# Performance work log

Hardware: AMD Instinct MI355X
Metric: run time of the kernel (lower is better)

Reference implementation:

```python
import jax, jax.numpy as jnp
import numpy as np

B, S, F, T = 32, 512, 512, 1024  # batch, seq_len(channel dim), feat_dim, time length


def setup_inputs() -> dict:
    key = jax.random.key(0)
    ks = jax.random.split(key, 6)
    scale = 0.05  # keep tanh/softmax in a non-saturated regime
    return {
        "z_robot": jax.random.normal(ks[0], (B, S, T), dtype=jnp.float32),
        "z_human": jax.random.normal(ks[1], (B, S, T), dtype=jnp.float32),
        "W_b": jax.random.normal(ks[2], (S, S), dtype=jnp.float32) * scale,
        "W_q": jax.random.normal(ks[3], (F, S), dtype=jnp.float32) * scale,
        "W_v": jax.random.normal(ks[4], (F, S), dtype=jnp.float32) * scale,
        "w_hq": jax.random.normal(ks[5], (1, F), dtype=jnp.float32) * scale,
    }


def reference(z_robot, z_human, W_b, W_q, W_v, w_hq):
    # aux = W_b @ z_human : [B, S, Th]
    aux = jnp.einsum('su,buh->bsh', W_b, z_human)
    # C = tanh(z_robot^T @ aux) : [B, Tr, Th]
    C = jnp.tanh(jnp.einsum('bst,bsh->bth', z_robot, aux))
    # aux2 = W_v @ z_human : [B, F, Th];  aux3 = W_q @ z_robot : [B, F, Tr]
    aux2 = jnp.einsum('fs,bsh->bfh', W_v, z_human)
    aux3 = jnp.einsum('fs,bst->bft', W_q, z_robot)
    # H_q = tanh(aux3 + aux2 @ C^T) : [B, F, Tr]
    H_q = jnp.tanh(aux3 + jnp.einsum('bfh,bth->bft', aux2, C))
    # a_q = softmax(w_hq @ H_q, axis=2) : [B, 1, Tr]
    a_q = jax.nn.softmax(jnp.einsum('of,bft->bot', w_hq, H_q), axis=2)
    # attn = z_robot @ a_q^T : [B, S, 1]
    attn = jnp.einsum('bst,bot->bso', z_robot, a_q)
    return (attn, a_q, C)
```

## Files before the change

### kernel.cpp

```cpp
#include <hip/hip_runtime.h>
#include <math.h>


using f32x4  = __attribute__((ext_vector_type(4))) float;
using bf16x8 = __attribute__((ext_vector_type(8))) short;

__device__ __forceinline__ ushort f2bf(float x) {
    uint u = __float_as_uint(x);
    return (ushort)((u + 0x7fffu + ((u >> 16) & 1u)) >> 16);
}
__device__ __forceinline__ float bf2f(ushort h) { return __uint_as_float((uint)h << 16); }

__device__ __forceinline__ float fast_tanh(float x) {
    return 1.0f - 2.0f / (__expf(2.0f * x) + 1.0f);
}

__device__ __forceinline__ void gll16(const void* g, void* l) {
    __builtin_amdgcn_global_load_lds(
        (__attribute__((address_space(1))) void*)(void*)g,
        (__attribute__((address_space(3))) void*)l, 16, 0, 0);
}


__global__ __launch_bounds__(256)
void transpose_split_k(const float* __restrict__ in, ushort* __restrict__ hi,
                       ushort* __restrict__ lo, int R, int Cn) {
    __shared__ float tile[32][33];
    const int b = blockIdx.z;
    const float* inb = in + (size_t)b * R * Cn;
    const int c0 = blockIdx.x * 32, r0 = blockIdx.y * 32;
    const int tx = threadIdx.x, ty = threadIdx.y;
    #pragma unroll
    for (int i = 0; i < 32; i += 8)
        tile[ty + i][tx] = inb[(size_t)(r0 + ty + i) * Cn + c0 + tx];
    __syncthreads();
    const size_t ob = (size_t)b * R * Cn;
    #pragma unroll
    for (int i = 0; i < 32; i += 8) {
        const float v = tile[tx][ty + i];
        const ushort h = f2bf(v);
        const size_t o = ob + (size_t)(c0 + ty + i) * R + r0 + tx;
        hi[o] = h;
        lo[o] = f2bf(v - bf2f(h));
    }
}

__global__ __launch_bounds__(256)
void convert_split_k(const float* __restrict__ in, ushort* __restrict__ hi,
                     ushort* __restrict__ lo, int n) {
    const int i = blockIdx.x * 256 + threadIdx.x;
    if (i < n) {
        const float v = in[i];
        const ushort h = f2bf(v);
        hi[i] = h;
        if (lo) lo[i] = f2bf(v - bf2f(h));
    }
}

template <int MODE>
__global__ __launch_bounds__(256, 2)
void gemm_split(const ushort* __restrict__ Ahi, const ushort* __restrict__ Alo,
                long sAb, int ldA,
                const ushort* __restrict__ Bhi, const ushort* __restrict__ Blo,
                long sBb, int ldB, int K,
                ushort* __restrict__ Ohi, ushort* __restrict__ Olo,
                float* __restrict__ Of, ushort* __restrict__ O16,
                int ldO, long sOb) {
    __shared__ __align__(16) ushort lds[32768];
    const int b = blockIdx.z, m0 = blockIdx.y * 128, n0 = blockIdx.x * 128;
    const int t = threadIdx.x, l = t & 63, w = t >> 6, wm = w >> 1, wn = w & 1;

    const int srow = l >> 2;
    const int sch  = ((l & 3) ^ (srow & 3)) * 8;
    const ushort* pAh = Ahi + (long)b * sAb + (long)(m0 + w * 32 + srow) * ldA + sch;
    const ushort* pAl = Alo + (long)b * sAb + (long)(m0 + w * 32 + srow) * ldA + sch;
    const ushort* pBh = Bhi + (long)b * sBb + (long)(n0 + w * 32 + srow) * ldB + sch;
    const ushort* pBl = Blo + (long)b * sBb + (long)(n0 + w * 32 + srow) * ldB + sch;

    const int q = l >> 4;
    int offA[4], offB[4];
    #pragma unroll
    for (int i = 0; i < 4; ++i) {
        const int rA = wm * 64 + i * 16 + (l & 15);
        offA[i] = rA * 32 + (q ^ (rA & 3)) * 8;
        const int rB = wn * 64 + i * 16 + (l & 15);
        offB[i] = rB * 32 + (q ^ (rB & 3)) * 8;
    }

    auto stage = [&](int k0, int st) {
        const int base = st * 16384;
        #pragma unroll
        for (int tt = 0; tt < 2; ++tt) {
            const int lo_ = base + (w * 32 + tt * 16) * 32;
            gll16(pAh + (long)(tt * 16) * ldA + k0, lds + lo_);
            gll16(pAl + (long)(tt * 16) * ldA + k0, lds + 4096 + lo_);
            gll16(pBh + (long)(tt * 16) * ldB + k0, lds + 8192 + lo_);
            gll16(pBl + (long)(tt * 16) * ldB + k0, lds + 12288 + lo_);
        }
    };

    f32x4 acc[4][4] = {};
    stage(0, 0);
    int st = 0;
    for (int k0 = 0; k0 < K; k0 += 32) {
        __syncthreads();
        if (k0 + 32 < K) stage(k0 + 32, st ^ 1);
        const int base = st * 16384;
        bf16x8 ah[4], al4[4], bh[4], bl4[4];
        #pragma unroll
        for (int i = 0; i < 4; ++i) {
            ah[i]  = *(const bf16x8*)&lds[base + offA[i]];
            al4[i] = *(const bf16x8*)&lds[base + 4096 + offA[i]];
            bh[i]  = *(const bf16x8*)&lds[base + 8192 + offB[i]];
            bl4[i] = *(const bf16x8*)&lds[base + 12288 + offB[i]];
        }
        #pragma unroll
        for (int i = 0; i < 4; ++i)
            #pragma unroll
            for (int j = 0; j < 4; ++j) {
                acc[i][j] = __builtin_amdgcn_mfma_f32_16x16x32_bf16(ah[i],  bh[j],  acc[i][j], 0, 0, 0);
                acc[i][j] = __builtin_amdgcn_mfma_f32_16x16x32_bf16(ah[i],  bl4[j], acc[i][j], 0, 0, 0);
                acc[i][j] = __builtin_amdgcn_mfma_f32_16x16x32_bf16(al4[i], bh[j],  acc[i][j], 0, 0, 0);
            }
        st ^= 1;
    }

    const int cl = l & 15, rl = (l >> 4) * 4;
    #pragma unroll
    for (int i = 0; i < 4; ++i)
        #pragma unroll
        for (int r = 0; r < 4; ++r) {
            const long mg = m0 + wm * 64 + i * 16 + rl + r;
            #pragma unroll
            for (int j = 0; j < 4; ++j) {
                const int ng = n0 + wn * 64 + j * 16 + cl;
                const float v = acc[i][j][r];
                const long o = (long)b * sOb + mg * ldO + ng;
                if (MODE == 0) {
                    const ushort h = f2bf(v);
                    Ohi[o] = h;
                    Olo[o] = f2bf(v - bf2f(h));
                } else {
                    const float tv = fast_tanh(v);
                    Of[o] = tv;
                    O16[o] = f2bf(tv);
                }
            }
        }
}

__device__ __forceinline__ void plain_core(
    const ushort* __restrict__ A, long sAb, int ldA,
    const ushort* __restrict__ B, long sBb, int ldB, int K,
    int b, int m0, int n0, ushort* lds, f32x4 (&acc)[4][4]) {
    const int t = threadIdx.x, l = t & 63, w = t >> 6, wm = w >> 1, wn = w & 1;
    const int srow = l >> 3;
    const int sch  = ((l & 7) ^ (srow & 7)) * 8;
    const ushort* pA = A + (long)b * sAb + (long)(m0 + w * 32 + srow) * ldA + sch;
    const ushort* pB = B + (long)b * sBb + (long)(n0 + w * 32 + srow) * ldB + sch;
    const int q = l >> 4;
    int offA[4], offB[4];
    #pragma unroll
    for (int i = 0; i < 4; ++i) {
        const int rA = wm * 64 + i * 16 + (l & 15);
        offA[i] = rA * 64 + (q ^ (rA & 7)) * 8;
        const int rB = wn * 64 + i * 16 + (l & 15);
        offB[i] = 8192 + rB * 64 + (q ^ (rB & 7)) * 8;
    }
    auto stage = [&](int k0, int st) {
        const int base = st * 16384;
        #pragma unroll
        for (int tt = 0; tt < 4; ++tt) {
            gll16(pA + (long)(tt * 8) * ldA + k0, lds + base + (w * 32 + tt * 8) * 64);
            gll16(pB + (long)(tt * 8) * ldB + k0, lds + base + 8192 + (w * 32 + tt * 8) * 64);
        }
    };
    stage(0, 0);
    int st = 0;
    for (int k0 = 0; k0 < K; k0 += 64) {
        __syncthreads();
        if (k0 + 64 < K) stage(k0 + 64, st ^ 1);
        const int base = st * 16384;
        #pragma unroll
        for (int s = 0; s < 2; ++s) {
            bf16x8 av[4], bv[4];
            #pragma unroll
            for (int i = 0; i < 4; ++i) {
                av[i] = *(const bf16x8*)&lds[base + (offA[i] ^ (s * 32))];
                bv[i] = *(const bf16x8*)&lds[base + (offB[i] ^ (s * 32))];
            }
            #pragma unroll
            for (int i = 0; i < 4; ++i)
                #pragma unroll
                for (int j = 0; j < 4; ++j)
                    acc[i][j] = __builtin_amdgcn_mfma_f32_16x16x32_bf16(av[i], bv[j], acc[i][j], 0, 0, 0);
        }
        st ^= 1;
    }
    __syncthreads();
}

__global__ __launch_bounds__(256, 2)
void gemm_plain_store(const ushort* __restrict__ A, long sAb, int ldA,
                      const ushort* __restrict__ B, long sBb, int ldB, int K,
                      ushort* __restrict__ O, long sOb, int ldO) {
    __shared__ __align__(16) ushort lds[32768];
    const int b = blockIdx.z, m0 = blockIdx.y * 128, n0 = blockIdx.x * 128;
    f32x4 acc[4][4] = {};
    plain_core(A, sAb, ldA, B, sBb, ldB, K, b, m0, n0, lds, acc);
    const int t = threadIdx.x, l = t & 63, w = t >> 6, wm = w >> 1, wn = w & 1;
    const int cl = l & 15, rl = (l >> 4) * 4;
    #pragma unroll
    for (int i = 0; i < 4; ++i)
        #pragma unroll
        for (int r = 0; r < 4; ++r) {
            const long mg = m0 + wm * 64 + i * 16 + rl + r;
            #pragma unroll
            for (int j = 0; j < 4; ++j)
                O[(long)b * sOb + mg * ldO + n0 + wn * 64 + j * 16 + cl] = f2bf(acc[i][j][r]);
        }
}

__global__ __launch_bounds__(256, 2)
void gemm_fused_logits(const ushort* __restrict__ Wq16, const ushort* __restrict__ zrT,
                       const ushort* __restrict__ aux2, const ushort* __restrict__ C16,
                       const float* __restrict__ whq, float* __restrict__ logits) {
    __shared__ __align__(16) ushort lds[32768];
    const int b = blockIdx.z, m0 = blockIdx.y * 128, n0 = blockIdx.x * 128;
    f32x4 acc[4][4] = {};
    plain_core(Wq16, 0, 512, zrT, 524288, 512, 512, b, m0, n0, lds, acc);
    plain_core(aux2, 524288, 1024, C16, 1048576, 1024, 1024, b, m0, n0, lds, acc);
    const int t = threadIdx.x, l = t & 63, w = t >> 6, wm = w >> 1, wn = w & 1;
    float p[4] = {0.f, 0.f, 0.f, 0.f};
    #pragma unroll
    for (int i = 0; i < 4; ++i)
        #pragma unroll
        for (int r = 0; r < 4; ++r) {
            const float wv = whq[m0 + wm * 64 + i * 16 + (l >> 4) * 4 + r];
            #pragma unroll
            for (int j = 0; j < 4; ++j)
                p[j] += wv * fast_tanh(acc[i][j][r]);
        }
    #pragma unroll
    for (int j = 0; j < 4; ++j) {
        p[j] += __shfl_xor(p[j], 16);
        p[j] += __shfl_xor(p[j], 32);
    }
    float* red = (float*)lds;
    if (l < 16) {
        #pragma unroll
        for (int j = 0; j < 4; ++j)
            red[wm * 128 + wn * 64 + j * 16 + l] = p[j];
    }
    __syncthreads();
    if (t < 128)
        atomicAdd(&logits[(long)b * 1024 + n0 + t], red[t] + red[128 + t]);
}

__global__ __launch_bounds__(256)
void softmax_kernel(const float* __restrict__ logits, float* __restrict__ aq, int T) {
    __shared__ float sm[256];
    const int b = blockIdx.x, tid = threadIdx.x;
    float v[4];
    float mx = -1e30f;
    #pragma unroll
    for (int i = 0; i < 4; ++i) {
        v[i] = logits[(size_t)b * T + tid + 256 * i];
        mx = fmaxf(mx, v[i]);
    }
    sm[tid] = mx; __syncthreads();
    for (int s = 128; s > 0; s >>= 1) {
        if (tid < s) sm[tid] = fmaxf(sm[tid], sm[tid + s]);
        __syncthreads();
    }
    mx = sm[0]; __syncthreads();
    float e[4], sum = 0.f;
    #pragma unroll
    for (int i = 0; i < 4; ++i) { e[i] = __expf(v[i] - mx); sum += e[i]; }
    sm[tid] = sum; __syncthreads();
    for (int s = 128; s > 0; s >>= 1) {
        if (tid < s) sm[tid] += sm[tid + s];
        __syncthreads();
    }
    const float inv = 1.0f / sm[0];
    #pragma unroll
    for (int i = 0; i < 4; ++i)
        aq[(size_t)b * T + tid + 256 * i] = e[i] * inv;
}

__global__ __launch_bounds__(256)
void attn_kernel(const float* __restrict__ ZR, const float* __restrict__ aq,
                 float* __restrict__ out, int S, int T) {
    const int b = blockIdx.y;
    const int s = blockIdx.x * 4 + (threadIdx.x >> 6);
    const int lane = threadIdx.x & 63;
    const float* row = ZR + ((size_t)b * S + s) * T;
    const float* a = aq + (size_t)b * T;
    float sum = 0.f;
    for (int t = lane; t < T; t += 64) sum += row[t] * a[t];
    #pragma unroll
    for (int off = 32; off > 0; off >>= 1) sum += __shfl_down(sum, off, 64);
    if (lane == 0) out[(size_t)b * S + s] = sum;
}

#define BM 64
#define BN 64
#define BK 16
#define PAD 4

__global__ __launch_bounds__(256)
void gemm_nn(const float* __restrict__ A, const float* __restrict__ Bm,
             float* __restrict__ D, int M, int N, int K) {
    __shared__ float As[BK][BM + PAD];
    __shared__ float Bs[BK][BN + PAD];
    const int b = blockIdx.z, m0 = blockIdx.y * BM, n0 = blockIdx.x * BN;
    const int tx = threadIdx.x, ty = threadIdx.y, f = ty * 16 + tx;
    const float* Bb = Bm + (size_t)b * K * N;
    float acc[4][4] = {};
    const int ka = f % 16, ma = f / 16, nb = f % 64, kb = f / 64;
    for (int k0 = 0; k0 < K; k0 += BK) {
        #pragma unroll
        for (int i = 0; i < 4; ++i)
            As[ka][ma + 16 * i] = A[(size_t)(m0 + ma + 16 * i) * K + k0 + ka];
        #pragma unroll
        for (int i = 0; i < 4; ++i)
            Bs[kb + 4 * i][nb] = Bb[(size_t)(k0 + kb + 4 * i) * N + n0 + nb];
        __syncthreads();
        #pragma unroll
        for (int k = 0; k < BK; ++k) {
            float av[4], bv[4];
            *(float4*)av = *(const float4*)&As[k][ty * 4];
            *(float4*)bv = *(const float4*)&Bs[k][tx * 4];
            #pragma unroll
            for (int i = 0; i < 4; ++i)
                #pragma unroll
                for (int j = 0; j < 4; ++j) acc[i][j] += av[i] * bv[j];
        }
        __syncthreads();
    }
    float* Db = D + (size_t)b * M * N;
    #pragma unroll
    for (int i = 0; i < 4; ++i)
        *(float4*)&Db[(size_t)(m0 + ty * 4 + i) * N + n0 + tx * 4] =
            make_float4(acc[i][0], acc[i][1], acc[i][2], acc[i][3]);
}

__global__ __launch_bounds__(256)
void gemm_tn_tanh(const float* __restrict__ ZR, const float* __restrict__ AUX,
                  float* __restrict__ C, int M, int N, int K) {
    __shared__ float As[BK][BM + PAD];
    __shared__ float Bs[BK][BN + PAD];
    const int b = blockIdx.z, m0 = blockIdx.y * BM, n0 = blockIdx.x * BN;
    const int tx = threadIdx.x, ty = threadIdx.y, f = ty * 16 + tx;
    const float* ZRb = ZR + (size_t)b * K * M;
    const float* AUXb = AUX + (size_t)b * K * N;
    float acc[4][4] = {};
    const int nl = f % 64, kl = f / 64;
    for (int k0 = 0; k0 < K; k0 += BK) {
        #pragma unroll
        for (int i = 0; i < 4; ++i)
            As[kl + 4 * i][nl] = ZRb[(size_t)(k0 + kl + 4 * i) * M + m0 + nl];
        #pragma unroll
        for (int i = 0; i < 4; ++i)
            Bs[kl + 4 * i][nl] = AUXb[(size_t)(k0 + kl + 4 * i) * N + n0 + nl];
        __syncthreads();
        #pragma unroll
        for (int k = 0; k < BK; ++k) {
            float av[4], bv[4];
            *(float4*)av = *(const float4*)&As[k][ty * 4];
            *(float4*)bv = *(const float4*)&Bs[k][tx * 4];
            #pragma unroll
            for (int i = 0; i < 4; ++i)
                #pragma unroll
                for (int j = 0; j < 4; ++j) acc[i][j] += av[i] * bv[j];
        }
        __syncthreads();
    }
    float* Cb = C + (size_t)b * M * N;
    #pragma unroll
    for (int i = 0; i < 4; ++i)
        *(float4*)&Cb[(size_t)(m0 + ty * 4 + i) * N + n0 + tx * 4] =
            make_float4(fast_tanh(acc[i][0]), fast_tanh(acc[i][1]),
                        fast_tanh(acc[i][2]), fast_tanh(acc[i][3]));
}

__global__ __launch_bounds__(256)
void gemm_nt_fused(const float* __restrict__ Wq, const float* __restrict__ ZR,
                   const float* __restrict__ A2, const float* __restrict__ Cm,
                   const float* __restrict__ whq, float* __restrict__ logits,
                   int M, int N, int K1, int K2) {
    __shared__ float As[BK][BM + PAD];
    __shared__ float Bs[BK][BN + PAD];
    __shared__ float red[16][BN];
    const int b = blockIdx.z, m0 = blockIdx.y * BM, n0 = blockIdx.x * BN;
    const int tx = threadIdx.x, ty = threadIdx.y, f = ty * 16 + tx;
    const float* ZRb = ZR + (size_t)b * K1 * N;
    const float* A2b = A2 + (size_t)b * M * K2;
    const float* Cb = Cm + (size_t)b * N * K2;
    float acc3[4][4] = {};
    {
        const int ka = f % 16, ma = f / 16, nb = f % 64, kb = f / 64;
        for (int k0 = 0; k0 < K1; k0 += BK) {
            #pragma unroll
            for (int i = 0; i < 4; ++i)
                As[ka][ma + 16 * i] = Wq[(size_t)(m0 + ma + 16 * i) * K1 + k0 + ka];
            #pragma unroll
            for (int i = 0; i < 4; ++i)
                Bs[kb + 4 * i][nb] = ZRb[(size_t)(k0 + kb + 4 * i) * N + n0 + nb];
            __syncthreads();
            #pragma unroll
            for (int k = 0; k < BK; ++k) {
                float av[4], bv[4];
                *(float4*)av = *(const float4*)&As[k][ty * 4];
                *(float4*)bv = *(const float4*)&Bs[k][tx * 4];
                #pragma unroll
                for (int i = 0; i < 4; ++i)
                    #pragma unroll
                    for (int j = 0; j < 4; ++j) acc3[i][j] += av[i] * bv[j];
            }
            __syncthreads();
        }
    }
    float acc[4][4] = {};
    {
        const int ka = f % 16, ra = f / 16;
        for (int k0 = 0; k0 < K2; k0 += BK) {
            #pragma unroll
            for (int i = 0; i < 4; ++i)
                As[ka][ra + 16 * i] = A2b[(size_t)(m0 + ra + 16 * i) * K2 + k0 + ka];
            #pragma unroll
            for (int i = 0; i < 4; ++i)
                Bs[ka][ra + 16 * i] = Cb[(size_t)(n0 + ra + 16 * i) * K2 + k0 + ka];
            __syncthreads();
            #pragma unroll
            for (int k = 0; k < BK; ++k) {
                float av[4], bv[4];
                *(float4*)av = *(const float4*)&As[k][ty * 4];
                *(float4*)bv = *(const float4*)&Bs[k][tx * 4];
                #pragma unroll
                for (int i = 0; i < 4; ++i)
                    #pragma unroll
                    for (int j = 0; j < 4; ++j) acc[i][j] += av[i] * bv[j];
            }
            __syncthreads();
        }
    }
    float p[4] = {0.f, 0.f, 0.f, 0.f};
    #pragma unroll
    for (int i = 0; i < 4; ++i) {
        const float wv = whq[m0 + ty * 4 + i];
        #pragma unroll
        for (int j = 0; j < 4; ++j) p[j] += wv * fast_tanh(acc3[i][j] + acc[i][j]);
    }
    #pragma unroll
    for (int j = 0; j < 4; ++j) red[ty][tx * 4 + j] = p[j];
    __syncthreads();
    if (f < BN) {
        float s = 0.f;
        #pragma unroll
        for (int r = 0; r < 16; ++r) s += red[r][f];
        atomicAdd(&logits[(size_t)b * N + n0 + f], s);
    }
}

extern "C" void kernel_launch(void* const* d_in, const int* in_sizes, int n_in,
                              void* d_out, int out_size, void* d_ws, size_t ws_size,
                              hipStream_t stream) {
    const float* z_robot = (const float*)d_in[0];
    const float* z_human = (const float*)d_in[1];
    const float* W_b     = (const float*)d_in[2];
    const float* W_q     = (const float*)d_in[3];
    const float* W_v     = (const float*)d_in[4];
    const float* w_hq    = (const float*)d_in[5];
    float* out = (float*)d_out;

    const int Bn = 32, S = 512, F = 512, T = 1024;
    float* attn_out = out;
    float* aq_out   = out + (size_t)Bn * S;
    float* C_out    = out + (size_t)Bn * S + (size_t)Bn * T;

    char* ws = (char*)d_ws;
    const size_t E2 = 33554432;

    ushort* zhT_hi  = (ushort*)(ws);
    ushort* zhT_lo  = (ushort*)(ws + E2);
    ushort* zrT_hi  = (ushort*)(ws + 2 * E2);
    ushort* zrT_lo  = (ushort*)(ws + 3 * E2);
    ushort* auxT_hi = (ushort*)(ws + 4 * E2);
    ushort* auxT_lo = (ushort*)(ws + 5 * E2);
    ushort* C16     = (ushort*)(ws + 6 * E2);
    ushort* aux2    = auxT_hi;
    ushort* Wb_hi   = (ushort*)(ws + 8 * E2);
    ushort* Wb_lo   = Wb_hi + 262144;
    ushort* Wq16    = Wb_hi + 524288;
    ushort* Wv16    = Wb_hi + 786432;
    float*  logitsF = (float*)(ws + 8 * E2 + 2097152);
    const size_t FAST_REQ = 8 * E2 + 2097152 + 131072;

    if (ws_size >= FAST_REQ) {
        hipMemsetAsync(logitsF, 0, (size_t)Bn * T * sizeof(float), stream);
        transpose_split_k<<<dim3(32, 16, Bn), dim3(32, 8), 0, stream>>>(z_human, zhT_hi, zhT_lo, 512, 1024);
        transpose_split_k<<<dim3(32, 16, Bn), dim3(32, 8), 0, stream>>>(z_robot, zrT_hi, zrT_lo, 512, 1024);
        convert_split_k<<<dim3(1024), dim3(256), 0, stream>>>(W_b, Wb_hi, Wb_lo, 262144);
        convert_split_k<<<dim3(1024), dim3(256), 0, stream>>>(W_q, Wq16, nullptr, 262144);
        convert_split_k<<<dim3(1024), dim3(256), 0, stream>>>(W_v, Wv16, nullptr, 262144);
        gemm_split<0><<<dim3(4, 8, Bn), dim3(256), 0, stream>>>(
            zhT_hi, zhT_lo, 524288, 512, Wb_hi, Wb_lo, 0, 512, 512,
            auxT_hi, auxT_lo, nullptr, nullptr, 512, 524288);
        gemm_split<1><<<dim3(8, 8, Bn), dim3(256), 0, stream>>>(
            zrT_hi, zrT_lo, 524288, 512, auxT_hi, auxT_lo, 524288, 512, 512,
            nullptr, nullptr, C_out, C16, 1024, 1048576);
        gemm_plain_store<<<dim3(8, 4, Bn), dim3(256), 0, stream>>>(
            Wv16, 0, 512, zhT_hi, 524288, 512, 512, aux2, 524288, 1024);
        gemm_fused_logits<<<dim3(8, 4, Bn), dim3(256), 0, stream>>>(
            Wq16, zrT_hi, aux2, C16, w_hq, logitsF);
        softmax_kernel<<<dim3(Bn), dim3(256), 0, stream>>>(logitsF, aq_out, T);
        attn_kernel<<<dim3(S / 4, Bn), dim3(256), 0, stream>>>(z_robot, aq_out, attn_out, S, T);
    } else {
        float* ws0    = (float*)ws;
        float* logits = (float*)(ws + (size_t)Bn * S * T * 4);
        hipMemsetAsync(logits, 0, (size_t)Bn * T * sizeof(float), stream);
        dim3 blk(16, 16);
        gemm_nn<<<dim3(T / BN, S / BM, Bn), blk, 0, stream>>>(W_b, z_human, ws0, S, T, S);
        gemm_tn_tanh<<<dim3(T / BN, T / BM, Bn), blk, 0, stream>>>(z_robot, ws0, C_out, T, T, S);
        gemm_nn<<<dim3(T / BN, F / BM, Bn), blk, 0, stream>>>(W_v, z_human, ws0, F, T, S);
        gemm_nt_fused<<<dim3(T / BN, F / BM, Bn), blk, 0, stream>>>(
            W_q, z_robot, ws0, C_out, w_hq, logits, F, T, S, T);
        softmax_kernel<<<dim3(Bn), dim3(256), 0, stream>>>(logits, aq_out, T);
        attn_kernel<<<dim3(S / 4, Bn), dim3(256), 0, stream>>>(z_robot, aq_out, attn_out, S, T);
    }
}
```

Baseline: 580.7 us.

## Remap GEMM blocks so each batch stays on one XCD, merge prep kernels

Changes every GEMM launch from a 3D grid to a 1D grid. A decode step assigns blocks so that all tiles of one batch land on the same XCD (id & 7), which lets that batch's operands be reused within one L2 instead of being spread across all eight. It also merges the two input transposes into one launch with wider 64-row tiles and packed ushort2 stores, and folds the three weight-conversion launches into one. The cost is integer div/mod per block and a decode that assumes the batch count is a multiple of 8.

After: 558.3 us. 1.04x faster.

```diff
diff --git a/kernel.cpp b/kernel.cpp
--- a/kernel.cpp
+++ b/kernel.cpp
@@ -21,39 +21,60 @@
         (__attribute__((address_space(3))) void*)l, 16, 0, 0);
 }
 
-
-__global__ __launch_bounds__(256)
-void transpose_split_k(const float* __restrict__ in, ushort* __restrict__ hi,
-                       ushort* __restrict__ lo, int R, int Cn) {
-    __shared__ float tile[32][33];
-    const int b = blockIdx.z;
-    const float* inb = in + (size_t)b * R * Cn;
-    const int c0 = blockIdx.x * 32, r0 = blockIdx.y * 32;
+__device__ __forceinline__ void xcd_decode(int id, int tiles_pb, int ntx,
+                                           int& batch, int& m0, int& n0) {
+    const int xcd = id & 7, slot = id >> 3;
+    batch = (slot / tiles_pb) * 8 + xcd;
+    const int tile = slot % tiles_pb;
+    m0 = (tile / ntx) * 128;
+    n0 = (tile % ntx) * 128;
+}
+
+
+__global__ __launch_bounds__(256)
+void transpose_split2_k(const float* __restrict__ inA, ushort* __restrict__ hiA,
+                        ushort* __restrict__ loA,
+                        const float* __restrict__ inB, ushort* __restrict__ hiB,
+                        ushort* __restrict__ loB) {
+    __shared__ float tile[32][65];
+    const int z = blockIdx.z;
+    const int b = z & 31, which = z >> 5;
+    const float* in = (which ? inB : inA) + (size_t)b * 512 * 1024;
+    ushort* hi = (which ? hiB : hiA) + (size_t)b * 512 * 1024;
+    ushort* lo = (which ? loB : loA) + (size_t)b * 512 * 1024;
+    const int c0 = blockIdx.x * 32, r0 = blockIdx.y * 64;
     const int tx = threadIdx.x, ty = threadIdx.y;
     #pragma unroll
-    for (int i = 0; i < 32; i += 8)
-        tile[ty + i][tx] = inb[(size_t)(r0 + ty + i) * Cn + c0 + tx];
+    for (int i = 0; i < 8; ++i)
+        tile[tx][ty + 8 * i] = in[(size_t)(r0 + ty + 8 * i) * 1024 + c0 + tx];
     __syncthreads();
-    const size_t ob = (size_t)b * R * Cn;
-    #pragma unroll
-    for (int i = 0; i < 32; i += 8) {
-        const float v = tile[tx][ty + i];
+    #pragma unroll
+    for (int j = 0; j < 4; ++j) {
+        const int c = ty + 8 * j;
+        const float v0 = tile[c][2 * tx], v1 = tile[c][2 * tx + 1];
+        const ushort h0 = f2bf(v0), h1 = f2bf(v1);
+        const size_t o = (size_t)(c0 + c) * 512 + r0 + 2 * tx;
+        *(ushort2*)&hi[o] = make_ushort2(h0, h1);
+        *(ushort2*)&lo[o] = make_ushort2(f2bf(v0 - bf2f(h0)), f2bf(v1 - bf2f(h1)));
+    }
+}
+
+__global__ __launch_bounds__(256)
+void convert_weights_k(const float* __restrict__ Wb, const float* __restrict__ Wq,
+                       const float* __restrict__ Wv, ushort* __restrict__ Wb_hi,
+                       ushort* __restrict__ Wb_lo, ushort* __restrict__ Wq16,
+                       ushort* __restrict__ Wv16) {
+    const int i = blockIdx.x * 256 + threadIdx.x;
+    const int seg = i >> 18, off = i & 262143;
+    if (seg == 0) {
+        const float v = Wb[off];
         const ushort h = f2bf(v);
-        const size_t o = ob + (size_t)(c0 + ty + i) * R + r0 + tx;
-        hi[o] = h;
-        lo[o] = f2bf(v - bf2f(h));
-    }
-}
-
-__global__ __launch_bounds__(256)
-void convert_split_k(const float* __restrict__ in, ushort* __restrict__ hi,
-                     ushort* __restrict__ lo, int n) {
-    const int i = blockIdx.x * 256 + threadIdx.x;
-    if (i < n) {
-        const float v = in[i];
-        const ushort h = f2bf(v);
-        hi[i] = h;
-        if (lo) lo[i] = f2bf(v - bf2f(h));
+        Wb_hi[off] = h;
+        Wb_lo[off] = f2bf(v - bf2f(h));
+    } else if (seg == 1) {
+        Wq16[off] = f2bf(Wq[off]);
+    } else {
+        Wv16[off] = f2bf(Wv[off]);
     }
 }
 
@@ -65,9 +86,10 @@
                 long sBb, int ldB, int K,
                 ushort* __restrict__ Ohi, ushort* __restrict__ Olo,
                 float* __restrict__ Of, ushort* __restrict__ O16,
-                int ldO, long sOb) {
+                int ldO, long sOb, int tiles_pb, int ntx) {
     __shared__ __align__(16) ushort lds[32768];
-    const int b = blockIdx.z, m0 = blockIdx.y * 128, n0 = blockIdx.x * 128;
+    int b, m0, n0;
+    xcd_decode(blockIdx.x, tiles_pb, ntx, b, m0, n0);
     const int t = threadIdx.x, l = t & 63, w = t >> 6, wm = w >> 1, wn = w & 1;
 
     const int srow = l >> 2;
@@ -203,9 +225,11 @@
 __global__ __launch_bounds__(256, 2)
 void gemm_plain_store(const ushort* __restrict__ A, long sAb, int ldA,
                       const ushort* __restrict__ B, long sBb, int ldB, int K,
-                      ushort* __restrict__ O, long sOb, int ldO) {
+                      ushort* __restrict__ O, long sOb, int ldO,
+                      int tiles_pb, int ntx) {
     __shared__ __align__(16) ushort lds[32768];
-    const int b = blockIdx.z, m0 = blockIdx.y * 128, n0 = blockIdx.x * 128;
+    int b, m0, n0;
+    xcd_decode(blockIdx.x, tiles_pb, ntx, b, m0, n0);
     f32x4 acc[4][4] = {};
     plain_core(A, sAb, ldA, B, sBb, ldB, K, b, m0, n0, lds, acc);
     const int t = threadIdx.x, l = t & 63, w = t >> 6, wm = w >> 1, wn = w & 1;
@@ -224,9 +248,11 @@
 __global__ __launch_bounds__(256, 2)
 void gemm_fused_logits(const ushort* __restrict__ Wq16, const ushort* __restrict__ zrT,
                        const ushort* __restrict__ aux2, const ushort* __restrict__ C16,
-                       const float* __restrict__ whq, float* __restrict__ logits) {
+                       const float* __restrict__ whq, float* __restrict__ logits,
+                       int tiles_pb, int ntx) {
     __shared__ __align__(16) ushort lds[32768];
-    const int b = blockIdx.z, m0 = blockIdx.y * 128, n0 = blockIdx.x * 128;
+    int b, m0, n0;
+    xcd_decode(blockIdx.x, tiles_pb, ntx, b, m0, n0);
     f32x4 acc[4][4] = {};
     plain_core(Wq16, 0, 512, zrT, 524288, 512, 512, b, m0, n0, lds, acc);
     plain_core(aux2, 524288, 1024, C16, 1048576, 1024, 1024, b, m0, n0, lds, acc);
@@ -474,7 +500,7 @@
     const float* w_hq    = (const float*)d_in[5];
     float* out = (float*)d_out;
 
-    const int Bn = 32, S = 512, F = 512, T = 1024;
+    const int Bn = 32, S = 512, T = 1024;
     float* attn_out = out;
     float* aq_out   = out + (size_t)Bn * S;
     float* C_out    = out + (size_t)Bn * S + (size_t)Bn * T;
@@ -499,21 +525,20 @@
 
     if (ws_size >= FAST_REQ) {
         hipMemsetAsync(logitsF, 0, (size_t)Bn * T * sizeof(float), stream);
-        transpose_split_k<<<dim3(32, 16, Bn), dim3(32, 8), 0, stream>>>(z_human, zhT_hi, zhT_lo, 512, 1024);
-        transpose_split_k<<<dim3(32, 16, Bn), dim3(32, 8), 0, stream>>>(z_robot, zrT_hi, zrT_lo, 512, 1024);
-        convert_split_k<<<dim3(1024), dim3(256), 0, stream>>>(W_b, Wb_hi, Wb_lo, 262144);
-        convert_split_k<<<dim3(1024), dim3(256), 0, stream>>>(W_q, Wq16, nullptr, 262144);
-        convert_split_k<<<dim3(1024), dim3(256), 0, stream>>>(W_v, Wv16, nullptr, 262144);
-        gemm_split<0><<<dim3(4, 8, Bn), dim3(256), 0, stream>>>(
+        transpose_split2_k<<<dim3(32, 8, 64), dim3(32, 8), 0, stream>>>(
+            z_human, zhT_hi, zhT_lo, z_robot, zrT_hi, zrT_lo);
+        convert_weights_k<<<dim3(3072), dim3(256), 0, stream>>>(
+            W_b, W_q, W_v, Wb_hi, Wb_lo, Wq16, Wv16);
+        gemm_split<0><<<dim3(32 * 32), dim3(256), 0, stream>>>(
             zhT_hi, zhT_lo, 524288, 512, Wb_hi, Wb_lo, 0, 512, 512,
-            auxT_hi, auxT_lo, nullptr, nullptr, 512, 524288);
-        gemm_split<1><<<dim3(8, 8, Bn), dim3(256), 0, stream>>>(
+            auxT_hi, auxT_lo, nullptr, nullptr, 512, 524288, 32, 4);
+        gemm_split<1><<<dim3(32 * 64), dim3(256), 0, stream>>>(
             zrT_hi, zrT_lo, 524288, 512, auxT_hi, auxT_lo, 524288, 512, 512,
-            nullptr, nullptr, C_out, C16, 1024, 1048576);
-        gemm_plain_store<<<dim3(8, 4, Bn), dim3(256), 0, stream>>>(
-            Wv16, 0, 512, zhT_hi, 524288, 512, 512, aux2, 524288, 1024);
-        gemm_fused_logits<<<dim3(8, 4, Bn), dim3(256), 0, stream>>>(
-            Wq16, zrT_hi, aux2, C16, w_hq, logitsF);
+            nullptr, nullptr, C_out, C16, 1024, 1048576, 64, 8);
+        gemm_plain_store<<<dim3(32 * 32), dim3(256), 0, stream>>>(
+            Wv16, 0, 512, zhT_hi, 524288, 512, 512, aux2, 524288, 1024, 32, 8);
+        gemm_fused_logits<<<dim3(32 * 32), dim3(256), 0, stream>>>(
+            Wq16, zrT_hi, aux2, C16, w_hq, logitsF, 32, 8);
         softmax_kernel<<<dim3(Bn), dim3(256), 0, stream>>>(logitsF, aq_out, T);
         attn_kernel<<<dim3(S / 4, Bn), dim3(256), 0, stream>>>(z_robot, aq_out, attn_out, S, T);
     } else {
@@ -523,9 +548,9 @@
         dim3 blk(16, 16);
         gemm_nn<<<dim3(T / BN, S / BM, Bn), blk, 0, stream>>>(W_b, z_human, ws0, S, T, S);
         gemm_tn_tanh<<<dim3(T / BN, T / BM, Bn), blk, 0, stream>>>(z_robot, ws0, C_out, T, T, S);
-        gemm_nn<<<dim3(T / BN, F / BM, Bn), blk, 0, stream>>>(W_v, z_human, ws0, F, T, S);
-        gemm_nt_fused<<<dim3(T / BN, F / BM, Bn), blk, 0, stream>>>(
-            W_q, z_robot, ws0, C_out, w_hq, logits, F, T, S, T);
+        gemm_nn<<<dim3(T / BN, 512 / BM, Bn), blk, 0, stream>>>(W_v, z_human, ws0, 512, T, S);
+        gemm_nt_fused<<<dim3(T / BN, 512 / BM, Bn), blk, 0, stream>>>(
+            W_q, z_robot, ws0, C_out, w_hq, logits, 512, T, S, T);
         softmax_kernel<<<dim3(Bn), dim3(256), 0, stream>>>(logits, aq_out, T);
         attn_kernel<<<dim3(S / 4, Bn), dim3(256), 0, stream>>>(z_robot, aq_out, attn_out, S, T);
     }
```
